# Performance work log

Measured on AMD Instinct MI355X. Metric: run time of the kernel, lower is better.

Reference implementation:

```python
import jax, jax.numpy as jnp
import numpy as np

B, S, D, H = 2, 2048, 1024, 16
HD = D // H  # 64
SOFT_CAP = 50.0
MAX_WAVELENGTH = 10000.0


def apply_rope(x, positions, head_dim):
    # x: [B,S,H,hd], positions: [B,S]
    fraction = 2.0 * jnp.arange(head_dim // 2, dtype=jnp.float32) / head_dim
    timescale = MAX_WAVELENGTH ** fraction                      # [hd/2]
    sinusoid = positions.astype(jnp.float32)[..., None] / timescale  # [B,S,hd/2]
    sin = jnp.sin(sinusoid)[..., None, :]                       # [B,S,1,hd/2]
    cos = jnp.cos(sinusoid)[..., None, :]
    first, second = jnp.split(x, 2, axis=-1)
    out = jnp.concatenate(
        [first * cos - second * sin, second * cos + first * sin], axis=-1)
    return out.astype(x.dtype)


def setup_inputs() -> dict:
    key = jax.random.key(0)
    k1, k2, k3 = jax.random.split(key, 3)
    inputs = jax.random.normal(k1, (B, S, D), jnp.float32)
    segment_positions = jnp.tile(jnp.arange(S, dtype=jnp.int32), (B, 1))
    mask = jnp.tril(jnp.ones((S, S), dtype=bool))[None, None]   # causal [1,1,S,S]
    w_in = jax.random.normal(k2, (D, H, 3 * HD), jnp.float32) * 0.02
    w_out = jax.random.normal(k3, (H, HD, D), jnp.float32) * 0.02
    return {"inputs": inputs, "segment_positions": segment_positions,
            "mask": mask, "w_in": w_in, "w_out": w_out}


def reference(inputs, segment_positions, mask, w_in, w_out):
    # fused QKV projection: [B,S,H,3*hd]
    proj = jnp.einsum('bsd,dhe->bshe', inputs, w_in)
    q, k, v = jnp.split(proj, 3, axis=-1)
    q = apply_rope(q, segment_positions, HD)
    k = apply_rope(k, segment_positions, HD)
    q = q / jnp.sqrt(jnp.float32(HD))
    attn = jnp.einsum('bqhd,bkhd->bhqk', q, k)                  # [B,H,S,S]
    big_neg = jnp.finfo(jnp.float32).min
    attn = jnp.where(mask, attn, big_neg)
    attn = jnp.tanh(attn / SOFT_CAP) * SOFT_CAP                 # soft-cap AFTER mask
    attn = jax.nn.softmax(attn, axis=-1)
    x = jnp.einsum('bhqk,bkhd->bqhd', attn, v)
    return jnp.einsum('bqhd,hdo->bqo', x, w_out)
```

## Files before the change

### kernel.cpp

```cpp
#include <hip/hip_runtime.h>
#include <math.h>

#define BB 2
#define SS 2048
#define DD 1024
#define HH 16
#define HDIM 64
#define BS (BB*SS)
#define NQKV (HH*3*HDIM)
#define PERHEAD ((size_t)SS*HDIM)

typedef __attribute__((ext_vector_type(8))) short bf16x8;
typedef __attribute__((ext_vector_type(4))) short bf16x4;
typedef __attribute__((ext_vector_type(4))) float f32x4;

typedef const __attribute__((address_space(1))) unsigned int ga_u32;
typedef __attribute__((address_space(3))) unsigned int lds_u32;

__device__ inline short f2bf(float x) {
    union { float f; unsigned u; } v; v.f = x;
    unsigned r = v.u + 0x7FFF + ((v.u >> 16) & 1);
    return (short)(r >> 16);
}

__device__ inline void gl_lds16(const void* g, void* l) {
    __builtin_amdgcn_global_load_lds((ga_u32*)g, (lds_u32*)l, 16, 0, 0);
}

__device__ inline f32x4 mfma16(bf16x4 a, bf16x4 b, f32x4 c) {
#if __has_builtin(__builtin_amdgcn_mfma_f32_16x16x16bf16_1k)
    return __builtin_amdgcn_mfma_f32_16x16x16bf16_1k(a, b, c, 0, 0, 0);
#else
    f32x4 d;
    asm("v_mfma_f32_16x16x16_bf16 %0, %1, %2, %3"
        : "=v"(d) : "v"(a), "v"(b), "v"(c));
    return d;
#endif
}

__global__ __launch_bounds__(256)
void setup_kernel(const float* __restrict__ A, unsigned short* __restrict__ Ab,
                  const int* __restrict__ pos, float2* __restrict__ tab,
                  const float* __restrict__ Win, unsigned short* __restrict__ Wtin,
                  const float* __restrict__ Wout, unsigned short* __restrict__ Wtout)
{
    __shared__ float tile[64][65];
    int bid = blockIdx.x, t = threadIdx.x;
    if (bid < 4096) {
        int i = (bid * 256 + t) * 4;
        float4 v = *(const float4*)&A[i];
        ushort4 o;
        o.x = (unsigned short)f2bf(v.x); o.y = (unsigned short)f2bf(v.y);
        o.z = (unsigned short)f2bf(v.z); o.w = (unsigned short)f2bf(v.w);
        *(ushort4*)&Ab[i] = o;
        return;
    }
    if (bid < 4608) {
        int idx = (bid - 4096) * 256 + t;
        int i = idx & 31, s = (idx >> 5) & 2047, b = idx >> 16;
        float p  = (float)pos[b * SS + s];
        float ts = powf(10000.0f, (float)i / 32.0f);
        float sn, cs;
        sincosf(p / ts, &sn, &cs);
        tab[idx] = make_float2(cs, sn);
        return;
    }
    const float* W; unsigned short* Wt; int K, N, tx, ty;
    if (bid < 5376) { int id = bid - 4608; W = Win;  Wt = Wtin;  K = DD; N = NQKV; tx = id % 48; ty = id / 48; }
    else            { int id = bid - 5376; W = Wout; Wt = Wtout; K = DD; N = DD;   tx = id % 16; ty = id / 16; }
    const int k0 = ty * 64, n0 = tx * 64;
    #pragma unroll
    for (int i = 0; i < 4; ++i) {
        int lin = t + 256 * i;
        int r = lin >> 4, c4 = (lin & 15) << 2;
        float4 v = *(const float4*)&W[(size_t)(k0 + r) * N + n0 + c4];
        tile[r][c4] = v.x; tile[r][c4 + 1] = v.y;
        tile[r][c4 + 2] = v.z; tile[r][c4 + 3] = v.w;
    }
    __syncthreads();
    #pragma unroll
    for (int i = 0; i < 4; ++i) {
        int lin = t + 256 * i;
        int n = lin >> 4, c4 = (lin & 15) << 2;
        ushort4 o;
        o.x = (unsigned short)f2bf(tile[c4 + 0][n]);
        o.y = (unsigned short)f2bf(tile[c4 + 1][n]);
        o.z = (unsigned short)f2bf(tile[c4 + 2][n]);
        o.w = (unsigned short)f2bf(tile[c4 + 3][n]);
        *(ushort4*)&Wt[(size_t)(n0 + n) * K + k0 + c4] = o;
    }
}

template<int QKV, int NT>
__global__ __launch_bounds__(256)
void gemm_mfma(const unsigned short* __restrict__ A,
               const unsigned short* __restrict__ Bt,
               float* __restrict__ C,
               unsigned short* __restrict__ Qb, unsigned short* __restrict__ Kb,
               unsigned short* __restrict__ Vb,
               const float2* __restrict__ tab,
               int M, int N, int K)
{
    __shared__ __align__(16) unsigned short As[128 * 32];
    __shared__ __align__(16) unsigned short Bs[NT * 32 * 32];
    const int t = threadIdx.x;
    const int wave = t >> 6, lane = t & 63;
    const int quad = lane >> 4, lc = lane & 15;
    const int bm = blockIdx.y * 128, bn = blockIdx.x * (NT * 32);
    const int wr = wave >> 1, wc = wave & 1;

    const int cb   = blockIdx.x * 2 + wc;
    const int h    = QKV ? (cb / 3) : 0;
    const int part = QKV ? (cb % 3) : 0;
    const bool vswap = QKV && (part == 2);

    const int r4 = lane >> 2;
    const int sc = (lane & 3) ^ ((lane >> 3) & 3);
    const unsigned short* aptr0 = A + (size_t)(bm + wave * 32 + r4) * K + sc * 8;
    const unsigned short* aptr1 = aptr0 + (size_t)16 * K;
    unsigned short* alds0 = &As[(wave * 32) * 32];
    unsigned short* alds1 = alds0 + 16 * 32;
    const unsigned short* bptr0 = Bt + (size_t)(bn + wave * (NT * 8) + r4) * K + sc * 8;
    const unsigned short* bptr1 = bptr0 + (size_t)16 * K;
    unsigned short* blds0 = &Bs[(wave * (NT * 8)) * 32];
    unsigned short* blds1 = blds0 + 16 * 32;

    const int cx = quad ^ ((lc >> 1) & 3);

    f32x4 acc[4][NT] = {};

    for (int k0 = 0; k0 < K; k0 += 32) {
        gl_lds16(aptr0 + k0, alds0);
        gl_lds16(aptr1 + k0, alds1);
        gl_lds16(bptr0 + k0, blds0);
        if (NT == 4) gl_lds16(bptr1 + k0, blds1);
        __syncthreads();

        bf16x8 af[4], bfr[NT];
        #pragma unroll
        for (int rt = 0; rt < 4; ++rt)
            af[rt] = *(const bf16x8*)&As[(wr * 64 + rt * 16 + lc) * 32 + cx * 8];
        #pragma unroll
        for (int nt = 0; nt < NT; ++nt)
            bfr[nt] = *(const bf16x8*)&Bs[(wc * (NT * 16) + nt * 16 + lc) * 32 + cx * 8];
        if (vswap) {
            #pragma unroll
            for (int rt = 0; rt < 4; ++rt)
                #pragma unroll
                for (int nt = 0; nt < NT; ++nt)
                    acc[rt][nt] = __builtin_amdgcn_mfma_f32_16x16x32_bf16(
                        bfr[nt], af[rt], acc[rt][nt], 0, 0, 0);
        } else {
            #pragma unroll
            for (int rt = 0; rt < 4; ++rt)
                #pragma unroll
                for (int nt = 0; nt < NT; ++nt)
                    acc[rt][nt] = __builtin_amdgcn_mfma_f32_16x16x32_bf16(
                        af[rt], bfr[nt], acc[rt][nt], 0, 0, 0);
        }
        __syncthreads();
    }

    if (QKV) {
        if (part == 2) {
            #pragma unroll
            for (int rt = 0; rt < 4; ++rt) {
                int m = bm + wr * 64 + rt * 16 + lc;
                int b = m >> 11, s = m & 2047;
                #pragma unroll
                for (int nt = 0; nt < 4; ++nt) {
                    #pragma unroll
                    for (int reg = 0; reg < 4; ++reg) {
                        int hd = nt * 16 + quad * 4 + reg;
                        Vb[(((size_t)(b * HH + h)) * HDIM + hd) * SS + s] =
                            (unsigned short)f2bf(acc[rt][nt][reg]);
                    }
                }
            }
        } else {
            unsigned short* dst = part == 0 ? Qb : Kb;
            const float scale = part == 0 ? 0.125f : 1.0f;
            #pragma unroll
            for (int rt = 0; rt < 4; ++rt) {
                #pragma unroll
                for (int reg = 0; reg < 4; ++reg) {
                    int m = bm + wr * 64 + rt * 16 + quad * 4 + reg;
                    int b = m >> 11, s = m & 2047;
                    size_t rowbase = (((size_t)(b * HH + h)) * SS + s) * HDIM;
                    #pragma unroll
                    for (int nt = 0; nt < 2; ++nt) {
                        int i = nt * 16 + lc;
                        float2 cssn = tab[((size_t)(b * SS + s)) * 32 + i];
                        float first  = acc[rt][nt][reg];
                        float second = acc[rt][nt + 2][reg];
                        dst[rowbase + i] =
                            (unsigned short)f2bf((first * cssn.x - second * cssn.y) * scale);
                        dst[rowbase + i + 32] =
                            (unsigned short)f2bf((second * cssn.x + first * cssn.y) * scale);
                    }
                }
            }
        }
    } else {
        #pragma unroll
        for (int rt = 0; rt < 4; ++rt)
            #pragma unroll
            for (int reg = 0; reg < 4; ++reg) {
                int m = bm + wr * 64 + rt * 16 + quad * 4 + reg;
                #pragma unroll
                for (int nt = 0; nt < NT; ++nt) {
                    int n = bn + wc * (NT * 16) + nt * 16 + lc;
                    C[(size_t)m * N + n] = acc[rt][nt][reg];
                }
            }
    }
}

__global__ __launch_bounds__(256)
void attn_mfma_kernel(const unsigned short* __restrict__ Qb,
                      const unsigned short* __restrict__ Kb,
                      const unsigned short* __restrict__ Vb,
                      unsigned short* __restrict__ Xb)
{
    __shared__ __align__(16) unsigned short Ks[2][64 * 64];
    __shared__ __align__(16) unsigned short Vs[2][64 * 64];

    const int t    = threadIdx.x;
    const int wave = t >> 6, lane = t & 63;
    const int quad = lane >> 4, lc = lane & 15;
    const int qt   = 31 - (blockIdx.x >> 5);
    const int bh   = blockIdx.x & 31;
    const int b    = bh >> 4, h = bh & 15;

    const unsigned short* Kbase = Kb + (size_t)bh * PERHEAD;
    const unsigned short* Vbase = Vb + (size_t)bh * PERHEAD;

    const int r8 = lane >> 3, c8 = lane & 7, gcs = c8 ^ r8;

    const unsigned short* Qbase =
        Qb + ((size_t)bh * SS + (size_t)(qt * 64 + wave * 16)) * HDIM;
    bf16x8 qf[2];
    qf[0] = *(const bf16x8*)&Qbase[lc * HDIM + quad * 8];
    qf[1] = *(const bf16x8*)&Qbase[lc * HDIM + 32 + quad * 8];

    f32x4 O[4] = {{0,0,0,0},{0,0,0,0},{0,0,0,0},{0,0,0,0}};
    f32x4 l_acc = {0.f, 0.f, 0.f, 0.f};
    const bf16x4 ones4 = {(short)0x3F80, (short)0x3F80, (short)0x3F80, (short)0x3F80};

    {
        const unsigned short* ks = Kbase + (size_t)(wave * 16 + r8) * HDIM + gcs * 8;
        gl_lds16(ks,            &Ks[0][(wave * 16)     * 64]);
        gl_lds16(ks + 8 * HDIM, &Ks[0][(wave * 16 + 8) * 64]);
        const unsigned short* vs = Vbase + (size_t)(wave * 16 + r8) * SS + gcs * 8;
        gl_lds16(vs,          &Vs[0][(wave * 16)     * 64]);
        gl_lds16(vs + 8 * SS, &Vs[0][(wave * 16 + 8) * 64]);
    }

    for (int kt = 0; kt <= qt; ++kt) {
        __syncthreads();
        const int buf = kt & 1;
        if (kt < qt) {
            const int nb = buf ^ 1;
            const unsigned short* ks =
                Kbase + (size_t)((kt + 1) * 64 + wave * 16 + r8) * HDIM + gcs * 8;
            gl_lds16(ks,            &Ks[nb][(wave * 16)     * 64]);
            gl_lds16(ks + 8 * HDIM, &Ks[nb][(wave * 16 + 8) * 64]);
            const unsigned short* vs =
                Vbase + (size_t)(wave * 16 + r8) * SS + (kt + 1) * 64 + gcs * 8;
            gl_lds16(vs,          &Vs[nb][(wave * 16)     * 64]);
            gl_lds16(vs + 8 * SS, &Vs[nb][(wave * 16 + 8) * 64]);
        }

        f32x4 St[4];
        #pragma unroll
        for (int kg = 0; kg < 4; ++kg) {
            St[kg] = (f32x4){0.f, 0.f, 0.f, 0.f};
            #pragma unroll
            for (int khd = 0; khd < 2; ++khd) {
                int pc = ((khd << 2) | quad) ^ (lc & 7);
                bf16x8 kf = *(const bf16x8*)&Ks[buf][(kg * 16 + lc) * 64 + pc * 8];
                St[kg] = __builtin_amdgcn_mfma_f32_16x16x32_bf16(
                    kf, qf[khd], St[kg], 0, 0, 0);
            }
        }

        const bool diag = (kt == qt);
        bf16x4 pf[4];
        #pragma unroll
        for (int kg = 0; kg < 4; ++kg) {
            unsigned up[4];
            #pragma unroll
            for (int reg = 0; reg < 4; ++reg) {
                float s  = St[kg][reg];
                float s2 = s * s;
                float u  = s * fmaf(s2, -1.92359339e-4f, 1.44269504f);
                float p  = __builtin_amdgcn_exp2f(u);
                if (diag && (kg * 16 + quad * 4 + reg > wave * 16 + lc)) p = 0.f;
                up[reg] = __builtin_bit_cast(unsigned, p) + 0x8000u;
            }
            uint2 pk;
            pk.x = __builtin_amdgcn_perm(up[1], up[0], 0x07060302);
            pk.y = __builtin_amdgcn_perm(up[3], up[2], 0x07060302);
            pf[kg] = __builtin_bit_cast(bf16x4, pk);
            l_acc = mfma16(pf[kg], ones4, l_acc);
        }

        #pragma unroll
        for (int g = 0; g < 4; ++g) {
            #pragma unroll
            for (int kg = 0; kg < 4; ++kg) {
                int pc2 = (kg * 2 + (quad >> 1)) ^ (lc & 7);
                bf16x4 vf = *(const bf16x4*)
                    &Vs[buf][(g * 16 + lc) * 64 + pc2 * 8 + (quad & 1) * 4];
                O[g] = mfma16(pf[kg], vf, O[g]);
            }
        }
    }

    #pragma unroll
    for (int reg = 0; reg < 4; ++reg) {
        float inv = __builtin_amdgcn_rcpf(l_acc[reg]);
        int q_g = qt * 64 + wave * 16 + quad * 4 + reg;
        size_t base = ((size_t)b * SS + q_g) * DD + h * HDIM;
        #pragma unroll
        for (int g = 0; g < 4; ++g)
            Xb[base + g * 16 + lc] = (unsigned short)f2bf(O[g][reg] * inv);
    }
}

extern "C" void kernel_launch(void* const* d_in, const int* in_sizes, int n_in,
                              void* d_out, int out_size, void* d_ws, size_t ws_size,
                              hipStream_t stream)
{
    const float* inputs = (const float*)d_in[0];
    const int*   pos    = (const int*)d_in[1];
    const float* w_in   = (const float*)d_in[3];
    const float* w_out  = (const float*)d_in[4];
    float* out = (float*)d_out;

    const size_t NELT = (size_t)BB * HH * SS * HDIM;
    unsigned short* Ab     = (unsigned short*)d_ws;
    unsigned short* Wt_in  = Ab + NELT;
    unsigned short* Wt_out = Wt_in + (size_t)NQKV * DD;
    unsigned short* Qb     = Wt_out + (size_t)DD * DD;
    unsigned short* Kb     = Qb + NELT;
    unsigned short* Vb     = Kb + NELT;
    unsigned short* Xb     = Vb + NELT;
    float2*         tab    = (float2*)(Xb + NELT);

    dim3 blk(256);
    setup_kernel<<<dim3(5632), blk, 0, stream>>>(
        inputs, Ab, pos, tab, w_in, Wt_in, w_out, Wt_out);
    gemm_mfma<1, 4><<<dim3(NQKV / 128, BS / 128), blk, 0, stream>>>(
        Ab, Wt_in, nullptr, Qb, Kb, Vb, tab, BS, NQKV, DD);
    attn_mfma_kernel<<<dim3(32 * BB * HH), blk, 0, stream>>>(Qb, Kb, Vb, Xb);
    gemm_mfma<0, 2><<<dim3(DD / 64, BS / 128), blk, 0, stream>>>(
        Xb, Wt_out, out, nullptr, nullptr, nullptr, nullptr, BS, DD, DD);
}
```

Baseline: 188.0 us.

## Peel diagonal tile out of attention loop and interleave q-tile block order

Moves the causal-masked diagonal key tile into a separate epilogue so the main loop has no mask test and no per-iteration prefetch branch. It also drops the +0x8000 rounding bias, so probabilities are truncated rather than rounded when packed to bf16. Block-to-q-tile mapping changes from strictly descending to an interleaved pattern (long, short, mid tiles mixed) to balance per-CU load across the causal triangle. The costs are more code size and slightly different numerics from the bf16 truncation.

```diff
diff --git a/kernel.cpp b/kernel.cpp
--- a/kernel.cpp
+++ b/kernel.cpp
@@ -228,7 +228,8 @@
     const int t    = threadIdx.x;
     const int wave = t >> 6, lane = t & 63;
     const int quad = lane >> 4, lc = lane & 15;
-    const int qt   = 31 - (blockIdx.x >> 5);
+    const int ord = blockIdx.x >> 5, g = ord & 7, grp = ord >> 3;
+    const int qt = (grp == 0) ? 31 - g : (grp == 1) ? g : (grp == 2) ? 23 - g : 8 + g;
     const int bh   = blockIdx.x & 31;
     const int b    = bh >> 4, h = bh & 15;
 
@@ -247,26 +248,24 @@
     f32x4 l_acc = {0.f, 0.f, 0.f, 0.f};
     const bf16x4 ones4 = {(short)0x3F80, (short)0x3F80, (short)0x3F80, (short)0x3F80};
 
+    const unsigned short* ksrc = Kbase + (size_t)(wave * 16 + r8) * HDIM + gcs * 8;
+    const unsigned short* vsrc = Vbase + (size_t)(wave * 16 + r8) * SS + gcs * 8;
+
     {
-        const unsigned short* ks = Kbase + (size_t)(wave * 16 + r8) * HDIM + gcs * 8;
-        gl_lds16(ks,            &Ks[0][(wave * 16)     * 64]);
-        gl_lds16(ks + 8 * HDIM, &Ks[0][(wave * 16 + 8) * 64]);
-        const unsigned short* vs = Vbase + (size_t)(wave * 16 + r8) * SS + gcs * 8;
-        gl_lds16(vs,          &Vs[0][(wave * 16)     * 64]);
-        gl_lds16(vs + 8 * SS, &Vs[0][(wave * 16 + 8) * 64]);
-    }
-
-    for (int kt = 0; kt <= qt; ++kt) {
+        gl_lds16(ksrc,            &Ks[0][(wave * 16)     * 64]);
+        gl_lds16(ksrc + 8 * HDIM, &Ks[0][(wave * 16 + 8) * 64]);
+        gl_lds16(vsrc,          &Vs[0][(wave * 16)     * 64]);
+        gl_lds16(vsrc + 8 * SS, &Vs[0][(wave * 16 + 8) * 64]);
+    }
+
+    for (int kt = 0; kt < qt; ++kt) {
         __syncthreads();
-        const int buf = kt & 1;
-        if (kt < qt) {
-            const int nb = buf ^ 1;
-            const unsigned short* ks =
-                Kbase + (size_t)((kt + 1) * 64 + wave * 16 + r8) * HDIM + gcs * 8;
+        const int buf = kt & 1, nb = buf ^ 1;
+        {
+            const unsigned short* ks = ksrc + (size_t)(kt + 1) * 64 * HDIM;
             gl_lds16(ks,            &Ks[nb][(wave * 16)     * 64]);
             gl_lds16(ks + 8 * HDIM, &Ks[nb][(wave * 16 + 8) * 64]);
-            const unsigned short* vs =
-                Vbase + (size_t)(wave * 16 + r8) * SS + (kt + 1) * 64 + gcs * 8;
+            const unsigned short* vs = vsrc + (kt + 1) * 64;
             gl_lds16(vs,          &Vs[nb][(wave * 16)     * 64]);
             gl_lds16(vs + 8 * SS, &Vs[nb][(wave * 16 + 8) * 64]);
         }
@@ -284,7 +283,6 @@
             }
         }
 
-        const bool diag = (kt == qt);
         bf16x4 pf[4];
         #pragma unroll
         for (int kg = 0; kg < 4; ++kg) {
@@ -292,11 +290,8 @@
             #pragma unroll
             for (int reg = 0; reg < 4; ++reg) {
                 float s  = St[kg][reg];
-                float s2 = s * s;
-                float u  = s * fmaf(s2, -1.92359339e-4f, 1.44269504f);
-                float p  = __builtin_amdgcn_exp2f(u);
-                if (diag && (kg * 16 + quad * 4 + reg > wave * 16 + lc)) p = 0.f;
-                up[reg] = __builtin_bit_cast(unsigned, p) + 0x8000u;
+                float u  = s * fmaf(s * s, -1.92359339e-4f, 1.44269504f);
+                up[reg]  = __builtin_bit_cast(unsigned, __builtin_amdgcn_exp2f(u));
             }
             uint2 pk;
             pk.x = __builtin_amdgcn_perm(up[1], up[0], 0x07060302);
@@ -306,13 +301,58 @@
         }
 
         #pragma unroll
-        for (int g = 0; g < 4; ++g) {
+        for (int gg = 0; gg < 4; ++gg) {
             #pragma unroll
             for (int kg = 0; kg < 4; ++kg) {
                 int pc2 = (kg * 2 + (quad >> 1)) ^ (lc & 7);
                 bf16x4 vf = *(const bf16x4*)
-                    &Vs[buf][(g * 16 + lc) * 64 + pc2 * 8 + (quad & 1) * 4];
-                O[g] = mfma16(pf[kg], vf, O[g]);
+                    &Vs[buf][(gg * 16 + lc) * 64 + pc2 * 8 + (quad & 1) * 4];
+                O[gg] = mfma16(pf[kg], vf, O[gg]);
+            }
+        }
+    }
+
+    {
+        __syncthreads();
+        const int buf = qt & 1;
+        f32x4 St[4];
+        #pragma unroll
+        for (int kg = 0; kg < 4; ++kg) {
+            St[kg] = (f32x4){0.f, 0.f, 0.f, 0.f};
+            #pragma unroll
+            for (int khd = 0; khd < 2; ++khd) {
+                int pc = ((khd << 2) | quad) ^ (lc & 7);
+                bf16x8 kf = *(const bf16x8*)&Ks[buf][(kg * 16 + lc) * 64 + pc * 8];
+                St[kg] = __builtin_amdgcn_mfma_f32_16x16x32_bf16(
+                    kf, qf[khd], St[kg], 0, 0, 0);
+            }
+        }
+        bf16x4 pf[4];
+        #pragma unroll
+        for (int kg = 0; kg < 4; ++kg) {
+            unsigned up[4];
+            #pragma unroll
+            for (int reg = 0; reg < 4; ++reg) {
+                float s  = St[kg][reg];
+                float u  = s * fmaf(s * s, -1.92359339e-4f, 1.44269504f);
+                float p  = __builtin_amdgcn_exp2f(u);
+                if (kg * 16 + quad * 4 + reg > wave * 16 + lc) p = 0.f;
+                up[reg]  = __builtin_bit_cast(unsigned, p);
+            }
+            uint2 pk;
+            pk.x = __builtin_amdgcn_perm(up[1], up[0], 0x07060302);
+            pk.y = __builtin_amdgcn_perm(up[3], up[2], 0x07060302);
+            pf[kg] = __builtin_bit_cast(bf16x4, pk);
+            l_acc = mfma16(pf[kg], ones4, l_acc);
+        }
+        #pragma unroll
+        for (int gg = 0; gg < 4; ++gg) {
+            #pragma unroll
+            for (int kg = 0; kg < 4; ++kg) {
+                int pc2 = (kg * 2 + (quad >> 1)) ^ (lc & 7);
+                bf16x4 vf = *(const bf16x4*)
+                    &Vs[buf][(gg * 16 + lc) * 64 + pc2 * 8 + (quad & 1) * 4];
+                O[gg] = mfma16(pf[kg], vf, O[gg]);
             }
         }
     }
@@ -323,8 +363,8 @@
         int q_g = qt * 64 + wave * 16 + quad * 4 + reg;
         size_t base = ((size_t)b * SS + q_g) * DD + h * HDIM;
         #pragma unroll
-        for (int g = 0; g < 4; ++g)
-            Xb[base + g * 16 + lc] = (unsigned short)f2bf(O[g][reg] * inv);
+        for (int gg = 0; gg < 4; ++gg)
+            Xb[base + gg * 16 + lc] = (unsigned short)f2bf(O[gg][reg] * inv);
     }
 }
 
```

Result: slower. 195.8 us (+4.1%).
